# Kernel tuning notes

Measured on AMD Instinct MI355X. Metric: run time of the kernel, lower is better.

The kernel has to match this reference:

```python
import jax, jax.numpy as jnp
import numpy as np

B, T, D, H = 2, 2048, 1024, 16
DH = D // H
TOPK = 64


def setup_inputs() -> dict:
    key = jax.random.key(0)
    ks = jax.random.split(key, 10)
    s = D ** -0.5
    x = jax.random.normal(ks[0], (B, T, D), dtype=jnp.float32)
    key_padding_mask = jax.random.bernoulli(ks[1], 0.1, (B, T))
    Wq = jax.random.normal(ks[2], (D, D), dtype=jnp.float32) * s
    bq = jnp.zeros((D,), dtype=jnp.float32)
    Wk = jax.random.normal(ks[3], (D, D), dtype=jnp.float32) * s
    bk = jnp.zeros((D,), dtype=jnp.float32)
    Wv = jax.random.normal(ks[4], (D, D), dtype=jnp.float32) * s
    bv = jnp.zeros((D,), dtype=jnp.float32)
    Wo = jax.random.normal(ks[5], (D, D), dtype=jnp.float32) * s
    bo = jnp.zeros((D,), dtype=jnp.float32)
    return {"x": x, "Wq": Wq, "bq": bq, "Wk": Wk, "bk": bk,
            "Wv": Wv, "bv": bv, "Wo": Wo, "bo": bo,
            "key_padding_mask": key_padding_mask, "causal": 1}


def _attention(x, Wq, bq, Wk, bk, Wv, bv, Wo, bo, key_padding_mask, causal):
    b, t, d = x.shape
    dh = d // H

    def heads(y):  # (B,T,D) -> (B,H,T,Dh)
        return y.reshape(b, t, H, dh).transpose(0, 2, 1, 3)

    q = heads(x @ Wq.T + bq)
    k = heads(x @ Wk.T + bk)
    v = heads(x @ Wv.T + bv)

    scale = dh ** -0.5
    logits = jnp.einsum('bhqd,bhkd->bhqk', q, k) * scale  # (B,H,T,T)
    neg = jnp.finfo(logits.dtype).min

    # key padding mask: True blocks key position
    logits = jnp.where(key_padding_mask[:, None, None, :], neg, logits)

    if causal:
        i = jnp.arange(t)[:, None]
        j = jnp.arange(t)[None, :]
        blocked = j > (t - t + i)  # Tq == Tk
        logits = jnp.where(blocked[None, None], neg, logits)

    # hard top-k sparsification: keep top-k logits per row, rest -> -inf
    flat = logits.reshape(-1, t)  # (B*H*T, T)
    vals, idx = jax.lax.top_k(flat, TOPK)
    rows = jnp.arange(flat.shape[0])[:, None]
    sparse = jnp.full_like(flat, neg).at[rows, idx].set(vals)
    sparse = sparse.reshape(logits.shape)

    attn = jax.nn.softmax(sparse, axis=-1)
    out = jnp.einsum('bhqk,bhkd->bhqd', attn, v)  # (B,H,T,Dh)
    out = out.transpose(0, 2, 1, 3).reshape(b, t, d)
    return out @ Wo.T + bo


def reference(x, Wq, bq, Wk, bk, Wv, bv, Wo, bo, key_padding_mask, causal):
    return _attention(x, Wq, bq, Wk, bk, Wv, bv, Wo, bo, key_padding_mask, causal)
```

## Files before the change

### kernel.cpp

```cpp
#include <hip/hip_runtime.h>
#include <hip/hip_bf16.h>
#include <stdint.h>

#define BB 2
#define TT 2048
#define DD 1024
#define NH 16
#define HD 64
#define TOPK 64
#define NEGF (-3.402823466e38f)
#define ORD_NEG 0x00800000u
#define QT 16
#define KT 256
#define SELCAP 96

typedef short short8x __attribute__((ext_vector_type(8)));
typedef float floatx4 __attribute__((ext_vector_type(4)));

__device__ __forceinline__ uint32_t ord_u32(float x) {
    uint32_t b = __float_as_uint(x);
    return (b & 0x80000000u) ? ~b : (b | 0x80000000u);
}
__device__ __forceinline__ float unord(uint32_t u) {
    uint32_t b = (u & 0x80000000u) ? (u ^ 0x80000000u) : ~u;
    return __uint_as_float(b);
}
__device__ __forceinline__ short bf16_rne(float x) {
    uint32_t u = __float_as_uint(x);
    u += 0x7FFFu + ((u >> 16) & 1u);
    return (short)(u >> 16);
}
__device__ __forceinline__ float bf16_to_f(short h) {
    return __uint_as_float(((uint32_t)(uint16_t)h) << 16);
}
__device__ __forceinline__ bool mask_at(const void* m, int mode, int idx) {
    if (mode == 0) return ((const int*)m)[idx] != 0;
    if (mode == 1) return ((const unsigned char*)m)[idx] != 0;
    return ((const float*)m)[idx] != 0.0f;
}

__device__ __forceinline__ int dpp_wsum(int v) {
    v += __builtin_amdgcn_update_dpp(0, v, 0x111, 0xf, 0xf, true);
    v += __builtin_amdgcn_update_dpp(0, v, 0x112, 0xf, 0xf, true);
    v += __builtin_amdgcn_update_dpp(0, v, 0x114, 0xf, 0xf, true);
    v += __builtin_amdgcn_update_dpp(0, v, 0x118, 0xf, 0xf, true);
    v += __builtin_amdgcn_update_dpp(0, v, 0x142, 0xa, 0xf, true);
    v += __builtin_amdgcn_update_dpp(0, v, 0x143, 0xc, 0xf, true);
    return __builtin_amdgcn_readlane(v, 63);
}
__device__ __forceinline__ uint32_t dpp_wumax(uint32_t v) {
    uint32_t t;
    t = (uint32_t)__builtin_amdgcn_update_dpp(0, (int)v, 0x111, 0xf, 0xf, true); v = v > t ? v : t;
    t = (uint32_t)__builtin_amdgcn_update_dpp(0, (int)v, 0x112, 0xf, 0xf, true); v = v > t ? v : t;
    t = (uint32_t)__builtin_amdgcn_update_dpp(0, (int)v, 0x114, 0xf, 0xf, true); v = v > t ? v : t;
    t = (uint32_t)__builtin_amdgcn_update_dpp(0, (int)v, 0x118, 0xf, 0xf, true); v = v > t ? v : t;
    t = (uint32_t)__builtin_amdgcn_update_dpp(0, (int)v, 0x142, 0xa, 0xf, true); v = v > t ? v : t;
    t = (uint32_t)__builtin_amdgcn_update_dpp(0, (int)v, 0x143, 0xc, 0xf, true); v = v > t ? v : t;
    return (uint32_t)__builtin_amdgcn_readlane((int)v, 63);
}
__device__ __forceinline__ float dpp_fsum(float v) {
    v += __uint_as_float((uint32_t)__builtin_amdgcn_update_dpp(0, (int)__float_as_uint(v), 0x111, 0xf, 0xf, true));
    v += __uint_as_float((uint32_t)__builtin_amdgcn_update_dpp(0, (int)__float_as_uint(v), 0x112, 0xf, 0xf, true));
    v += __uint_as_float((uint32_t)__builtin_amdgcn_update_dpp(0, (int)__float_as_uint(v), 0x114, 0xf, 0xf, true));
    v += __uint_as_float((uint32_t)__builtin_amdgcn_update_dpp(0, (int)__float_as_uint(v), 0x118, 0xf, 0xf, true));
    v += __uint_as_float((uint32_t)__builtin_amdgcn_update_dpp(0, (int)__float_as_uint(v), 0x142, 0xa, 0xf, true));
    v += __uint_as_float((uint32_t)__builtin_amdgcn_update_dpp(0, (int)__float_as_uint(v), 0x143, 0xc, 0xf, true));
    return __uint_as_float((uint32_t)__builtin_amdgcn_readlane((int)__float_as_uint(v), 63));
}

__global__ void __launch_bounds__(1024) build_flags(
    const unsigned char* raw, const int* causalp, int* flags, uint32_t* Mt)
{
    __shared__ int odd_nz, big, s_mode;
    __shared__ uint32_t smt[BB * 64];
    const int tid = threadIdx.x;
    if (tid == 0) { odd_nz = 0; big = 0; }
    if (tid < BB * 64) smt[tid] = 0;
    __syncthreads();
    for (int i = tid; i < BB * TT; i += 1024) {
        unsigned char c = raw[i];
        if ((i & 3) && c) atomicOr(&odd_nz, 1);
        if (c > 1) atomicOr(&big, 1);
    }
    __syncthreads();
    if (tid == 0) {
        int mode = odd_nz ? (big ? 2 : 1) : 0;
        s_mode = mode;
        flags[0] = mode;
        flags[1] = (causalp[0] != 0) ? 1 : 0;
    }
    __syncthreads();
    const int mode = s_mode;
    const int w = tid >> 3, g = tid & 7;
    const int bb = w >> 6, l = w & 63;
    uint32_t bits = 0;
#pragma unroll
    for (int si = 0; si < 4; ++si) {
        int s = g * 4 + si;
        if (mask_at(raw, mode, bb * TT + l + 64 * s)) bits |= (1u << s);
    }
    if (bits) atomicOr(&smt[w], bits);
    __syncthreads();
    if (tid < BB * 64) Mt[tid] = smt[tid];
}

__global__ void __launch_bounds__(256) split_f32(
    const float* __restrict__ in, short* __restrict__ hi, short* __restrict__ lo,
    int n4, float scale)
{
    int i = blockIdx.x * blockDim.x + threadIdx.x;
    if (i >= n4) return;
    float4 v = ((const float4*)in)[i];
    float f[4] = {v.x * scale, v.y * scale, v.z * scale, v.w * scale};
    short hh[4], ll[4];
#pragma unroll
    for (int j = 0; j < 4; ++j) {
        hh[j] = bf16_rne(f[j]);
        ll[j] = bf16_rne(f[j] - bf16_to_f(hh[j]));
    }
    short4 h4; h4.x = hh[0]; h4.y = hh[1]; h4.z = hh[2]; h4.w = hh[3];
    short4 l4; l4.x = ll[0]; l4.y = ll[1]; l4.z = ll[2]; l4.w = ll[3];
    ((short4*)hi)[i] = h4;
    ((short4*)lo)[i] = l4;
}

__global__ void __launch_bounds__(256) split_w4(
    const float* __restrict__ W0, const float* __restrict__ W1,
    const float* __restrict__ W2, const float* __restrict__ W3,
    short* __restrict__ h0, short* __restrict__ l0, short* __restrict__ h1, short* __restrict__ l1,
    short* __restrict__ h2, short* __restrict__ l2, short* __restrict__ h3, short* __restrict__ l3,
    int n4)
{
    int i = blockIdx.x * blockDim.x + threadIdx.x;
    if (i >= n4) return;
    const int w = blockIdx.y;
    const float* in = (w == 0) ? W0 : (w == 1) ? W1 : (w == 2) ? W2 : W3;
    short* hi = (w == 0) ? h0 : (w == 1) ? h1 : (w == 2) ? h2 : h3;
    short* lo = (w == 0) ? l0 : (w == 1) ? l1 : (w == 2) ? l2 : l3;
    float4 v = ((const float4*)in)[i];
    float f[4] = {v.x, v.y, v.z, v.w};
    short hh[4], ll[4];
#pragma unroll
    for (int j = 0; j < 4; ++j) {
        hh[j] = bf16_rne(f[j]);
        ll[j] = bf16_rne(f[j] - bf16_to_f(hh[j]));
    }
    short4 h4; h4.x = hh[0]; h4.y = hh[1]; h4.z = hh[2]; h4.w = hh[3];
    short4 l4; l4.x = ll[0]; l4.y = ll[1]; l4.z = ll[2]; l4.w = ll[3];
    ((short4*)hi)[i] = h4;
    ((short4*)lo)[i] = l4;
}

__global__ void __launch_bounds__(256) gemm_bf16s(
    const short* __restrict__ Ah, const short* __restrict__ Al,
    const short* __restrict__ Bh, const short* __restrict__ Bl,
    const float* __restrict__ bias, float* __restrict__ Cf,
    short* __restrict__ Ch, short* __restrict__ Cl, float scale, int mode)
{
    const int bid = blockIdx.x;
    const int xcd = bid & 7, slot = bid >> 3;
    const int panel = xcd * 4 + (slot >> 4);
    const int ncol  = slot & 15;
    const int tid = threadIdx.x, lane = tid & 63, wv = tid >> 6;
    const int wr = wv >> 1, wc = wv & 1;
    const int m0 = panel * 128 + wr * 64;
    const int n0 = ncol * 64 + wc * 32;
    const int lrow = lane & 15, lk = (lane >> 4) * 8;

    floatx4 acc[4][2];
#pragma unroll
    for (int i = 0; i < 4; ++i)
#pragma unroll
        for (int j = 0; j < 2; ++j) acc[i][j] = (floatx4){0.f, 0.f, 0.f, 0.f};

    auto ldfr = [&](int kk, short8x* pah, short8x* pal, short8x* pbh, short8x* pbl) {
#pragma unroll
        for (int mb = 0; mb < 4; ++mb) {
            size_t off = (size_t)(m0 + mb * 16 + lrow) * DD + kk + lk;
            pah[mb] = *(const short8x*)(Ah + off);
            pal[mb] = *(const short8x*)(Al + off);
        }
#pragma unroll
        for (int nb = 0; nb < 2; ++nb) {
            size_t off = (size_t)(n0 + nb * 16 + lrow) * DD + kk + lk;
            pbh[nb] = *(const short8x*)(Bh + off);
            pbl[nb] = *(const short8x*)(Bl + off);
        }
    };
    auto domfma = [&](short8x* pah, short8x* pal, short8x* pbh, short8x* pbl) {
#pragma unroll
        for (int mb = 0; mb < 4; ++mb)
#pragma unroll
            for (int nb = 0; nb < 2; ++nb) {
                acc[mb][nb] = __builtin_amdgcn_mfma_f32_16x16x32_bf16(pah[mb], pbh[nb], acc[mb][nb], 0, 0, 0);
                acc[mb][nb] = __builtin_amdgcn_mfma_f32_16x16x32_bf16(pah[mb], pbl[nb], acc[mb][nb], 0, 0, 0);
                acc[mb][nb] = __builtin_amdgcn_mfma_f32_16x16x32_bf16(pal[mb], pbh[nb], acc[mb][nb], 0, 0, 0);
            }
    };

    short8x A0[4], L0[4], B0[2], C0[2];
    short8x A1[4], L1[4], B1[2], C1[2];
    ldfr(0, A0, L0, B0, C0);
    for (int kk = 0; kk < DD; kk += 64) {
        ldfr(kk + 32, A1, L1, B1, C1);
        domfma(A0, L0, B0, C0);
        if (kk + 64 < DD) ldfr(kk + 64, A0, L0, B0, C0);
        domfma(A1, L1, B1, C1);
    }

#pragma unroll
    for (int mb = 0; mb < 4; ++mb)
#pragma unroll
        for (int nb = 0; nb < 2; ++nb) {
            int n = n0 + nb * 16 + lrow;
            float bv = bias[n];
#pragma unroll
            for (int j = 0; j < 4; ++j) {
                int m = m0 + mb * 16 + (lane >> 4) * 4 + j;
                float v = acc[mb][nb][j] + bv;
                if (mode == 0) {
                    Cf[(size_t)m * DD + n] = v;
                } else {
                    int b = m >> 11, t = m & (TT - 1), h = n >> 6, dh = n & (HD - 1);
                    size_t idx = (((size_t)b * NH + h) * TT + t) * HD + dh;
                    if (mode == 1) {
                        Cf[idx] = v;
                    } else {
                        v *= scale;
                        short hi16 = bf16_rne(v);
                        Ch[idx] = hi16;
                        Cl[idx] = bf16_rne(v - bf16_to_f(hi16));
                    }
                }
            }
        }
}

__global__ void __launch_bounds__(256) gemm_xwt(
    const float* __restrict__ A, const float* __restrict__ W,
    const float* __restrict__ bias, float* __restrict__ C,
    int M, int N, int K, int split_heads)
{
    __shared__ float As[64][17];
    __shared__ float Ws[64][17];
    const int tid = threadIdx.x;
    const int tx = tid & 15, ty = tid >> 4;
    const int arow = blockIdx.y * 64, bcol = blockIdx.x * 64;
    float acc[4][4] = {};

    for (int k0 = 0; k0 < K; k0 += 16) {
        const int r = tid >> 2, c = (tid & 3) * 4;
        float4 a4 = *(const float4*)(A + (size_t)(arow + r) * K + k0 + c);
        As[r][c] = a4.x; As[r][c + 1] = a4.y; As[r][c + 2] = a4.z; As[r][c + 3] = a4.w;
        float4 w4 = *(const float4*)(W + (size_t)(bcol + r) * K + k0 + c);
        Ws[r][c] = w4.x; Ws[r][c + 1] = w4.y; Ws[r][c + 2] = w4.z; Ws[r][c + 3] = w4.w;
        __syncthreads();
#pragma unroll
        for (int k = 0; k < 16; ++k) {
            float a0 = As[ty * 4 + 0][k], a1 = As[ty * 4 + 1][k];
            float a2 = As[ty * 4 + 2][k], a3 = As[ty * 4 + 3][k];
            float w0 = Ws[tx * 4 + 0][k], w1 = Ws[tx * 4 + 1][k];
            float w2 = Ws[tx * 4 + 2][k], w3 = Ws[tx * 4 + 3][k];
            acc[0][0] += a0 * w0; acc[0][1] += a0 * w1; acc[0][2] += a0 * w2; acc[0][3] += a0 * w3;
            acc[1][0] += a1 * w0; acc[1][1] += a1 * w1; acc[1][2] += a1 * w2; acc[1][3] += a1 * w3;
            acc[2][0] += a2 * w0; acc[2][1] += a2 * w1; acc[2][2] += a2 * w2; acc[2][3] += a2 * w3;
            acc[3][0] += a3 * w0; acc[3][1] += a3 * w1; acc[3][2] += a3 * w2; acc[3][3] += a3 * w3;
        }
        __syncthreads();
    }

#pragma unroll
    for (int i = 0; i < 4; ++i) {
        int m = arow + ty * 4 + i;
#pragma unroll
        for (int j = 0; j < 4; ++j) {
            int n = bcol + tx * 4 + j;
            float v = acc[i][j] + bias[n];
            if (split_heads) {
                int b = m / TT, t = m % TT, h = n / HD, dh = n % HD;
                C[(((size_t)b * NH + h) * TT + t) * HD + dh] = v;
            } else {
                C[(size_t)m * N + n] = v;
            }
        }
    }
}

__global__ void __launch_bounds__(1024) attn_topk(
    const short* __restrict__ Qhi, const short* __restrict__ Qlo,
    const short* __restrict__ Khi, const short* __restrict__ Klo,
    const float* __restrict__ V, const uint32_t* __restrict__ Mt,
    const int* __restrict__ flags, short* __restrict__ Ohi,
    short* __restrict__ Olo, float* __restrict__ Of)
{
    __shared__ float s_S[2][QT][KT + 1];
    __shared__ int2  s_sel[QT][SELCAP];

    const int tid = threadIdx.x, lane = tid & 63, wv = tid >> 6;
    const int d = blockIdx.x;
    const int xcd = d & 7, chunk = d >> 3;
    const int bh = (xcd << 2) | (chunk >> 7);
    const int qt = chunk & 127;
    const int b = bh >> 4, h = bh & 15;
    const int causal = flags[1];
    const size_t hb = (size_t)bh * (size_t)TT * HD;
    const int r0 = qt * QT;
    const int gq = r0 + wv;
    const float* __restrict__ Vh = V + hb;
    const float* __restrict__ Vl = Vh + lane;

    short8x qhi[2], qlo[2];
    {
        const size_t qoff = hb + (size_t)(r0 + (lane & 15)) * HD + (lane >> 4) * 8;
        qhi[0] = *(const short8x*)(Qhi + qoff);
        qhi[1] = *(const short8x*)(Qhi + qoff + 32);
        qlo[0] = *(const short8x*)(Qlo + qoff);
        qlo[1] = *(const short8x*)(Qlo + qoff + 32);
    }

    const uint32_t mwords = Mt[b * 64 + lane];

    uint32_t lgo[32];
#pragma unroll
    for (int i = 0; i < 32; ++i) lgo[i] = ORD_NEG;

    const int lastT = causal ? ((r0 + QT - 1) >> 8) : 7;

#pragma unroll
    for (int t = 0; t < 8; ++t) {
        if (t <= lastT) {
            const size_t koff = hb + (size_t)(t * KT + wv * 16 + (lane & 15)) * HD + (lane >> 4) * 8;
            short8x kh0 = *(const short8x*)(Khi + koff);
            short8x kh1 = *(const short8x*)(Khi + koff + 32);
            short8x kl0 = *(const short8x*)(Klo + koff);
            short8x kl1 = *(const short8x*)(Klo + koff + 32);
            floatx4 acc = {0.f, 0.f, 0.f, 0.f};
            acc = __builtin_amdgcn_mfma_f32_16x16x32_bf16(qhi[0], kh0, acc, 0, 0, 0);
            acc = __builtin_amdgcn_mfma_f32_16x16x32_bf16(qhi[0], kl0, acc, 0, 0, 0);
            acc = __builtin_amdgcn_mfma_f32_16x16x32_bf16(qlo[0], kh0, acc, 0, 0, 0);
            acc = __builtin_amdgcn_mfma_f32_16x16x32_bf16(qhi[1], kh1, acc, 0, 0, 0);
            acc = __builtin_amdgcn_mfma_f32_16x16x32_bf16(qhi[1], kl1, acc, 0, 0, 0);
            acc = __builtin_amdgcn_mfma_f32_16x16x32_bf16(qlo[1], kh1, acc, 0, 0, 0);
#pragma unroll
            for (int j = 0; j < 4; ++j)
                s_S[t & 1][(lane >> 4) * 4 + j][wv * 16 + (lane & 15)] = acc[j];
            __syncthreads();
#pragma unroll
            for (int j = 0; j < 4; ++j) {
                float sv = s_S[t & 1][wv][j * 64 + lane];
                int key = t * KT + j * 64 + lane;
                bool blocked = ((mwords >> (t * 4 + j)) & 1u) || (causal && key > gq);
                lgo[t * 4 + j] = blocked ? ORD_NEG : ord_u32(sv);
            }
        }
    }

    uint32_t moL = 0;
#pragma unroll
    for (int i = 0; i < 32; ++i) {
        uint32_t u = lgo[i];
        moL = u > moL ? u : moL;
    }
    const uint32_t mo = dpp_wumax(moL);

    auto wcount = [&](uint32_t thrv) -> int {
        int c = 0;
#pragma unroll
        for (int i = 0; i < 32; ++i) c += (lgo[i] >= thrv) ? 1 : 0;
        return dpp_wsum(c);
    };

    float outv;
    if (mo == ORD_NEG) {
        float a0 = 0.f, a1 = 0.f, a2 = 0.f, a3 = 0.f;
        for (int j = 0; j < TT; j += 4) {
            a0 += Vh[(j + 0) * HD + lane];
            a1 += Vh[(j + 1) * HD + lane];
            a2 += Vh[(j + 2) * HD + lane];
            a3 += Vh[(j + 3) * HD + lane];
        }
        outv = (a0 + a1 + a2 + a3) * (1.0f / TT);
    } else {
        const float mF = unord(mo);
        uint32_t thr = 0; uint32_t lo_b = 0, hi_b = 0; int done = 0;
        {
            uint32_t p1 = ord_u32(mF - 2.0f);
            int c1 = wcount(p1);
            if (c1 == TOPK) { thr = p1; done = 1; }
            else if (c1 > TOPK) { lo_b = p1; hi_b = mo; }
            else {
                uint32_t p2 = ord_u32(mF - 4.0f);
                int c2 = wcount(p2);
                if (c2 == TOPK) { thr = p2; done = 1; }
                else if (c2 > TOPK) { lo_b = p2; hi_b = p1; }
                else {
                    uint32_t p3 = ord_u32(mF - 15.0f);
                    int c3 = wcount(p3);
                    if (c3 <= TOPK) { thr = p3; done = 1; }
                    else { lo_b = p3; hi_b = p2; }
                }
            }
        }
        if (!done) {
            while (hi_b - lo_b > 1u) {
                uint32_t mid = lo_b + ((hi_b - lo_b) >> 1);
                int c = wcount(mid);
                if (c == TOPK) { lo_b = mid; break; }
                if (c > TOPK) lo_b = mid; else hi_b = mid;
            }
            thr = lo_b;
        }

        float Sp = 0.f;
#pragma unroll
        for (int i = 0; i < 32; ++i) {
            uint32_t u = lgo[i];
            float w = 0.f;
            if (u >= thr) w = __expf(unord(u) - mF);
            Sp += w;
            lgo[i] = (w > 0.f) ? __float_as_uint(w) : 0u;
        }
        const float S = dpp_fsum(Sp);

        int base = 0;
#pragma unroll
        for (int i = 0; i < 32; ++i) {
            uint32_t wbits = lgo[i];
            unsigned long long msk = __ballot(wbits != 0);
            if (wbits) {
                int below = __builtin_amdgcn_mbcnt_hi((uint32_t)(msk >> 32),
                            __builtin_amdgcn_mbcnt_lo((uint32_t)msk, 0));
                int pos = base + below;
                if (pos < SELCAP) {
                    int keyoff = (((i >> 2) * KT + (i & 3) * 64 + lane) << 6);
                    s_sel[wv][pos] = make_int2(keyoff, (int)wbits);
                }
            }
            base += (int)__popcll(msk);
        }
        int cnt = base < SELCAP ? base : SELCAP;

        float acc = 0.f;
        int i2 = 0;
        for (; i2 + 4 <= cnt; i2 += 4) {
            int2 e0 = s_sel[wv][i2],     e1 = s_sel[wv][i2 + 1];
            int2 e2 = s_sel[wv][i2 + 2], e3 = s_sel[wv][i2 + 3];
            int k0 = __builtin_amdgcn_readfirstlane(e0.x);
            int k1 = __builtin_amdgcn_readfirstlane(e1.x);
            int k2 = __builtin_amdgcn_readfirstlane(e2.x);
            int k3 = __builtin_amdgcn_readfirstlane(e3.x);
            float w0 = __uint_as_float((uint32_t)__builtin_amdgcn_readfirstlane(e0.y));
            float w1 = __uint_as_float((uint32_t)__builtin_amdgcn_readfirstlane(e1.y));
            float w2 = __uint_as_float((uint32_t)__builtin_amdgcn_readfirstlane(e2.y));
            float w3 = __uint_as_float((uint32_t)__builtin_amdgcn_readfirstlane(e3.y));
            acc += w0 * Vl[k0];
            acc += w1 * Vl[k1];
            acc += w2 * Vl[k2];
            acc += w3 * Vl[k3];
        }
        for (; i2 < cnt; ++i2) {
            int2 e = s_sel[wv][i2];
            int k = __builtin_amdgcn_readfirstlane(e.x);
            float w = __uint_as_float((uint32_t)__builtin_amdgcn_readfirstlane(e.y));
            acc += w * Vl[k];
        }
        outv = acc / S;
    }
    const size_t oidx = ((size_t)b * TT + gq) * DD + h * HD + lane;
    if (Of) {
        Of[oidx] = outv;
    } else {
        short hi16 = bf16_rne(outv);
        Ohi[oidx] = hi16;
        Olo[oidx] = bf16_rne(outv - bf16_to_f(hi16));
    }
}

extern "C" void kernel_launch(void* const* d_in, const int* in_sizes, int n_in,
                              void* d_out, int out_size, void* d_ws, size_t ws_size,
                              hipStream_t stream) {
    const float* x  = (const float*)d_in[0];
    const float* Wq = (const float*)d_in[1];
    const float* bq = (const float*)d_in[2];
    const float* Wk = (const float*)d_in[3];
    const float* bk = (const float*)d_in[4];
    const float* Wv = (const float*)d_in[5];
    const float* bv = (const float*)d_in[6];
    const float* Wo = (const float*)d_in[7];
    const float* bo = (const float*)d_in[8];
    const void*  maskp = d_in[9];
    const int*   causalp = (const int*)d_in[10];
    float* out = (float*)d_out;

    char* ws = (char*)d_ws;
    const size_t TEN  = (size_t)BB * TT * DD * sizeof(float);
    const size_t HTEN = TEN / 2;
    const size_t WSZ  = (size_t)DD * DD * 2;
    const size_t NEED = 6 * TEN + 4096;

    const int nx4 = BB * TT * DD / 4, nw4 = DD * DD / 4;

    if (ws_size >= NEED) {
        float* Vf   = (float*)(ws);
        short* xh   = (short*)(ws + TEN);
        short* xl   = (short*)(ws + TEN + HTEN);
        short* Qhi  = (short*)(ws + 2 * TEN);
        short* Qlo  = (short*)(ws + 2 * TEN + HTEN);
        short* Khi  = (short*)(ws + 3 * TEN);
        short* Klo  = (short*)(ws + 3 * TEN + HTEN);
        short* Ohi  = (short*)(ws + 4 * TEN);
        short* Olo  = (short*)(ws + 4 * TEN + HTEN);
        char*  wb   = ws + 5 * TEN;
        short* wqh = (short*)(wb);            short* wql = (short*)(wb + WSZ);
        short* wkh = (short*)(wb + 2 * WSZ);  short* wkl = (short*)(wb + 3 * WSZ);
        short* wvh = (short*)(wb + 4 * WSZ);  short* wvl = (short*)(wb + 5 * WSZ);
        short* woh = (short*)(wb + 6 * WSZ);  short* wol = (short*)(wb + 7 * WSZ);
        int*      flags = (int*)(wb + 8 * WSZ);
        uint32_t* Mt    = (uint32_t*)(wb + 8 * WSZ + 256);

        build_flags<<<1, 1024, 0, stream>>>((const unsigned char*)maskp, causalp, flags, Mt);

        split_f32<<<(nx4 + 255) / 256, 256, 0, stream>>>(x, xh, xl, nx4, 1.0f);
        dim3 wg((nw4 + 255) / 256, 4);
        split_w4<<<wg, 256, 0, stream>>>(Wq, Wk, Wv, Wo,
                                         wqh, wql, wkh, wkl, wvh, wvl, woh, wol, nw4);

        gemm_bf16s<<<512, 256, 0, stream>>>(xh, xl, wqh, wql, bq, nullptr, Qhi, Qlo, 0.125f, 2);
        gemm_bf16s<<<512, 256, 0, stream>>>(xh, xl, wkh, wkl, bk, nullptr, Khi, Klo, 1.0f, 2);
        gemm_bf16s<<<512, 256, 0, stream>>>(xh, xl, wvh, wvl, bv, Vf, nullptr, nullptr, 1.0f, 1);

        attn_topk<<<BB * NH * (TT / QT), 1024, 0, stream>>>(Qhi, Qlo, Khi, Klo, Vf, Mt, flags,
                                                            Ohi, Olo, nullptr);

        gemm_bf16s<<<512, 256, 0, stream>>>(Ohi, Olo, woh, wol, bo, out, nullptr, nullptr, 1.0f, 0);
    } else {
        float* Qf  = (float*)(ws);
        float* Kf  = (float*)(ws + TEN);
        float* Vf  = (float*)(ws + 2 * TEN);
        float* O   = (float*)(ws + 3 * TEN);
        short* Qhi = (short*)(ws + 4 * TEN);
        short* Qlo = (short*)(ws + 4 * TEN + HTEN);
        short* Khi = (short*)(ws + 5 * TEN);
        short* Klo = (short*)(ws + 5 * TEN + HTEN);
        int*      flags = (int*)(ws + 6 * TEN);
        uint32_t* Mt    = (uint32_t*)(ws + 6 * TEN + 256);

        build_flags<<<1, 1024, 0, stream>>>((const unsigned char*)maskp, causalp, flags, Mt);
        dim3 g2(DD / 64, (BB * TT) / 64);
        gemm_xwt<<<g2, 256, 0, stream>>>(x, Wq, bq, Qf, BB * TT, DD, DD, 1);
        gemm_xwt<<<g2, 256, 0, stream>>>(x, Wk, bk, Kf, BB * TT, DD, DD, 1);
        gemm_xwt<<<g2, 256, 0, stream>>>(x, Wv, bv, Vf, BB * TT, DD, DD, 1);
        split_f32<<<(nx4 + 255) / 256, 256, 0, stream>>>(Qf, Qhi, Qlo, nx4, 0.125f);
        split_f32<<<(nx4 + 255) / 256, 256, 0, stream>>>(Kf, Khi, Klo, nx4, 1.0f);
        attn_topk<<<BB * NH * (TT / QT), 1024, 0, stream>>>(Qhi, Qlo, Khi, Klo, Vf, Mt, flags,
                                                            nullptr, nullptr, O);
        gemm_xwt<<<g2, 256, 0, stream>>>(O, Wo, bo, out, BB * TT, DD, DD, 0);
    }
}
```

Before: 770.4 us.

## Fuse QKV GEMMs, drop split-bf16 for V and output projections

Merges the three Q/K/V projection GEMMs into one 1536-block launch. The V projection and the output projection now use a single bf16 MFMA term instead of the three-term hi/lo split, and the attention output is stored as bf16 only. In the attention kernel the count uses ballot/popcount, and the softmax weights are computed only for the selected keys, with weights and keys held in registers and read back via readlane instead of broadcast LDS reads. This cuts MFMA work and memory traffic in two of the GEMMs, at the cost of lower precision in the V and output projections.

```diff
diff --git a/kernel.cpp b/kernel.cpp
--- a/kernel.cpp
+++ b/kernel.cpp
@@ -39,15 +39,6 @@
     return ((const float*)m)[idx] != 0.0f;
 }
 
-__device__ __forceinline__ int dpp_wsum(int v) {
-    v += __builtin_amdgcn_update_dpp(0, v, 0x111, 0xf, 0xf, true);
-    v += __builtin_amdgcn_update_dpp(0, v, 0x112, 0xf, 0xf, true);
-    v += __builtin_amdgcn_update_dpp(0, v, 0x114, 0xf, 0xf, true);
-    v += __builtin_amdgcn_update_dpp(0, v, 0x118, 0xf, 0xf, true);
-    v += __builtin_amdgcn_update_dpp(0, v, 0x142, 0xa, 0xf, true);
-    v += __builtin_amdgcn_update_dpp(0, v, 0x143, 0xc, 0xf, true);
-    return __builtin_amdgcn_readlane(v, 63);
-}
 __device__ __forceinline__ uint32_t dpp_wumax(uint32_t v) {
     uint32_t t;
     t = (uint32_t)__builtin_amdgcn_update_dpp(0, (int)v, 0x111, 0xf, 0xf, true); v = v > t ? v : t;
@@ -151,11 +142,104 @@
     ((short4*)lo)[i] = l4;
 }
 
+__global__ void __launch_bounds__(256) gemm_qkv(
+    const short* __restrict__ Ah, const short* __restrict__ Al,
+    const short* __restrict__ Wqh, const short* __restrict__ Wql,
+    const short* __restrict__ Wkh, const short* __restrict__ Wkl,
+    const short* __restrict__ Wvh,
+    const float* __restrict__ bq, const float* __restrict__ bk, const float* __restrict__ bv,
+    short* __restrict__ Qhi, short* __restrict__ Qlo,
+    short* __restrict__ Khi, short* __restrict__ Klo, float* __restrict__ Vf)
+{
+    const int bid = blockIdx.x;
+    const int xcd = bid & 7, slot = bid >> 3;
+    const int panel = xcd * 4 + slot / 48;
+    const int nc48  = slot % 48;
+    const int wsel  = nc48 >> 4;
+    const int ncol  = nc48 & 15;
+    const int tid = threadIdx.x, lane = tid & 63, wv = tid >> 6;
+    const int wr = wv >> 1, wc = wv & 1;
+    const int m0 = panel * 128 + wr * 64;
+    const int n0 = ncol * 64 + wc * 32;
+    const int lrow = lane & 15, lk = (lane >> 4) * 8;
+
+    const short* Bh = (wsel == 0) ? Wqh : (wsel == 1) ? Wkh : Wvh;
+    const short* Bl = (wsel == 0) ? Wql : Wkl;
+    const float* bias = (wsel == 0) ? bq : (wsel == 1) ? bk : bv;
+    const int terms = (wsel == 2) ? 0 : 3;
+
+    floatx4 acc[4][2];
+#pragma unroll
+    for (int i = 0; i < 4; ++i)
+#pragma unroll
+        for (int j = 0; j < 2; ++j) acc[i][j] = (floatx4){0.f, 0.f, 0.f, 0.f};
+
+    auto ldfr = [&](int kk, short8x* pah, short8x* pal, short8x* pbh, short8x* pbl) {
+#pragma unroll
+        for (int mb = 0; mb < 4; ++mb) {
+            size_t off = (size_t)(m0 + mb * 16 + lrow) * DD + kk + lk;
+            pah[mb] = *(const short8x*)(Ah + off);
+            if (terms) pal[mb] = *(const short8x*)(Al + off);
+        }
+#pragma unroll
+        for (int nb = 0; nb < 2; ++nb) {
+            size_t off = (size_t)(n0 + nb * 16 + lrow) * DD + kk + lk;
+            pbh[nb] = *(const short8x*)(Bh + off);
+            if (terms) pbl[nb] = *(const short8x*)(Bl + off);
+        }
+    };
+    auto domfma = [&](short8x* pah, short8x* pal, short8x* pbh, short8x* pbl) {
+#pragma unroll
+        for (int mb = 0; mb < 4; ++mb)
+#pragma unroll
+            for (int nb = 0; nb < 2; ++nb) {
+                acc[mb][nb] = __builtin_amdgcn_mfma_f32_16x16x32_bf16(pah[mb], pbh[nb], acc[mb][nb], 0, 0, 0);
+                if (terms) {
+                    acc[mb][nb] = __builtin_amdgcn_mfma_f32_16x16x32_bf16(pah[mb], pbl[nb], acc[mb][nb], 0, 0, 0);
+                    acc[mb][nb] = __builtin_amdgcn_mfma_f32_16x16x32_bf16(pal[mb], pbh[nb], acc[mb][nb], 0, 0, 0);
+                }
+            }
+    };
+
+    short8x A0[4], L0[4], B0[2], C0[2];
+    short8x A1[4], L1[4], B1[2], C1[2];
+    ldfr(0, A0, L0, B0, C0);
+    for (int kk = 0; kk < DD; kk += 64) {
+        ldfr(kk + 32, A1, L1, B1, C1);
+        domfma(A0, L0, B0, C0);
+        if (kk + 64 < DD) ldfr(kk + 64, A0, L0, B0, C0);
+        domfma(A1, L1, B1, C1);
+    }
+
+    const float scale = (wsel == 0) ? 0.125f : 1.0f;
+#pragma unroll
+    for (int mb = 0; mb < 4; ++mb)
+#pragma unroll
+        for (int nb = 0; nb < 2; ++nb) {
+            int n = n0 + nb * 16 + lrow;
+            float bv2 = bias[n];
+#pragma unroll
+            for (int j = 0; j < 4; ++j) {
+                int m = m0 + mb * 16 + (lane >> 4) * 4 + j;
+                float v = acc[mb][nb][j] + bv2;
+                int b = m >> 11, t = m & (TT - 1), h = n >> 6, dh = n & (HD - 1);
+                size_t idx = (((size_t)b * NH + h) * TT + t) * HD + dh;
+                if (wsel == 2) {
+                    Vf[idx] = v;
+                } else {
+                    v *= scale;
+                    short hi16 = bf16_rne(v);
+                    short lo16 = bf16_rne(v - bf16_to_f(hi16));
+                    if (wsel == 0) { Qhi[idx] = hi16; Qlo[idx] = lo16; }
+                    else           { Khi[idx] = hi16; Klo[idx] = lo16; }
+                }
+            }
+        }
+}
+
 __global__ void __launch_bounds__(256) gemm_bf16s(
-    const short* __restrict__ Ah, const short* __restrict__ Al,
-    const short* __restrict__ Bh, const short* __restrict__ Bl,
-    const float* __restrict__ bias, float* __restrict__ Cf,
-    short* __restrict__ Ch, short* __restrict__ Cl, float scale, int mode)
+    const short* __restrict__ Ah, const short* __restrict__ Bh,
+    const float* __restrict__ bias, float* __restrict__ Cf)
 {
     const int bid = blockIdx.x;
     const int xcd = bid & 7, slot = bid >> 3;
@@ -173,39 +257,29 @@
 #pragma unroll
         for (int j = 0; j < 2; ++j) acc[i][j] = (floatx4){0.f, 0.f, 0.f, 0.f};
 
-    auto ldfr = [&](int kk, short8x* pah, short8x* pal, short8x* pbh, short8x* pbl) {
-#pragma unroll
-        for (int mb = 0; mb < 4; ++mb) {
-            size_t off = (size_t)(m0 + mb * 16 + lrow) * DD + kk + lk;
-            pah[mb] = *(const short8x*)(Ah + off);
-            pal[mb] = *(const short8x*)(Al + off);
-        }
-#pragma unroll
-        for (int nb = 0; nb < 2; ++nb) {
-            size_t off = (size_t)(n0 + nb * 16 + lrow) * DD + kk + lk;
-            pbh[nb] = *(const short8x*)(Bh + off);
-            pbl[nb] = *(const short8x*)(Bl + off);
-        }
+    auto ldfr = [&](int kk, short8x* pah, short8x* pbh) {
+#pragma unroll
+        for (int mb = 0; mb < 4; ++mb)
+            pah[mb] = *(const short8x*)(Ah + (size_t)(m0 + mb * 16 + lrow) * DD + kk + lk);
+#pragma unroll
+        for (int nb = 0; nb < 2; ++nb)
+            pbh[nb] = *(const short8x*)(Bh + (size_t)(n0 + nb * 16 + lrow) * DD + kk + lk);
     };
-    auto domfma = [&](short8x* pah, short8x* pal, short8x* pbh, short8x* pbl) {
+    auto domfma = [&](short8x* pah, short8x* pbh) {
 #pragma unroll
         for (int mb = 0; mb < 4; ++mb)
 #pragma unroll
-            for (int nb = 0; nb < 2; ++nb) {
+            for (int nb = 0; nb < 2; ++nb)
                 acc[mb][nb] = __builtin_amdgcn_mfma_f32_16x16x32_bf16(pah[mb], pbh[nb], acc[mb][nb], 0, 0, 0);
-                acc[mb][nb] = __builtin_amdgcn_mfma_f32_16x16x32_bf16(pah[mb], pbl[nb], acc[mb][nb], 0, 0, 0);
-                acc[mb][nb] = __builtin_amdgcn_mfma_f32_16x16x32_bf16(pal[mb], pbh[nb], acc[mb][nb], 0, 0, 0);
-            }
     };
 
-    short8x A0[4], L0[4], B0[2], C0[2];
-    short8x A1[4], L1[4], B1[2], C1[2];
-    ldfr(0, A0, L0, B0, C0);
+    short8x A0[4], B0[2], A1[4], B1[2];
+    ldfr(0, A0, B0);
     for (int kk = 0; kk < DD; kk += 64) {
-        ldfr(kk + 32, A1, L1, B1, C1);
-        domfma(A0, L0, B0, C0);
-        if (kk + 64 < DD) ldfr(kk + 64, A0, L0, B0, C0);
-        domfma(A1, L1, B1, C1);
+        ldfr(kk + 32, A1, B1);
+        domfma(A0, B0);
+        if (kk + 64 < DD) ldfr(kk + 64, A0, B0);
+        domfma(A1, B1);
     }
 
 #pragma unroll
@@ -217,21 +291,7 @@
 #pragma unroll
             for (int j = 0; j < 4; ++j) {
                 int m = m0 + mb * 16 + (lane >> 4) * 4 + j;
-                float v = acc[mb][nb][j] + bv;
-                if (mode == 0) {
-                    Cf[(size_t)m * DD + n] = v;
-                } else {
-                    int b = m >> 11, t = m & (TT - 1), h = n >> 6, dh = n & (HD - 1);
-                    size_t idx = (((size_t)b * NH + h) * TT + t) * HD + dh;
-                    if (mode == 1) {
-                        Cf[idx] = v;
-                    } else {
-                        v *= scale;
-                        short hi16 = bf16_rne(v);
-                        Ch[idx] = hi16;
-                        Cl[idx] = bf16_rne(v - bf16_to_f(hi16));
-                    }
-                }
+                Cf[(size_t)m * DD + n] = acc[mb][nb][j] + bv;
             }
         }
 }
@@ -291,7 +351,7 @@
     const short* __restrict__ Khi, const short* __restrict__ Klo,
     const float* __restrict__ V, const uint32_t* __restrict__ Mt,
     const int* __restrict__ flags, short* __restrict__ Ohi,
-    short* __restrict__ Olo, float* __restrict__ Of)
+    float* __restrict__ Of)
 {
     __shared__ float s_S[2][QT][KT + 1];
     __shared__ int2  s_sel[QT][SELCAP];
@@ -366,8 +426,9 @@
     auto wcount = [&](uint32_t thrv) -> int {
         int c = 0;
 #pragma unroll
-        for (int i = 0; i < 32; ++i) c += (lgo[i] >= thrv) ? 1 : 0;
-        return dpp_wsum(c);
+        for (int i = 0; i < 32; ++i)
+            c += (int)__popcll(__ballot(lgo[i] >= thrv));
+        return c;
     };
 
     float outv;
@@ -411,69 +472,69 @@
             thr = lo_b;
         }
 
-        float Sp = 0.f;
+        int base = 0;
 #pragma unroll
         for (int i = 0; i < 32; ++i) {
             uint32_t u = lgo[i];
-            float w = 0.f;
-            if (u >= thr) w = __expf(unord(u) - mF);
-            Sp += w;
-            lgo[i] = (w > 0.f) ? __float_as_uint(w) : 0u;
-        }
-        const float S = dpp_fsum(Sp);
-
-        int base = 0;
-#pragma unroll
-        for (int i = 0; i < 32; ++i) {
-            uint32_t wbits = lgo[i];
-            unsigned long long msk = __ballot(wbits != 0);
-            if (wbits) {
+            unsigned long long msk = __ballot(u >= thr);
+            if (u >= thr) {
                 int below = __builtin_amdgcn_mbcnt_hi((uint32_t)(msk >> 32),
                             __builtin_amdgcn_mbcnt_lo((uint32_t)msk, 0));
                 int pos = base + below;
                 if (pos < SELCAP) {
                     int keyoff = (((i >> 2) * KT + (i & 3) * 64 + lane) << 6);
-                    s_sel[wv][pos] = make_int2(keyoff, (int)wbits);
+                    s_sel[wv][pos] = make_int2(keyoff, (int)u);
                 }
             }
             base += (int)__popcll(msk);
         }
-        int cnt = base < SELCAP ? base : SELCAP;
+        const int cnt = base < SELCAP ? base : SELCAP;
+
+        float w0r = 0.f, w1r = 0.f; int key0r = 0, key1r = 0;
+        if (lane < cnt) {
+            int2 e = s_sel[wv][lane];
+            key0r = e.x;
+            w0r = __expf(unord((uint32_t)e.y) - mF);
+        }
+        if (64 + lane < cnt) {
+            int2 e = s_sel[wv][64 + lane];
+            key1r = e.x;
+            w1r = __expf(unord((uint32_t)e.y) - mF);
+        }
+        const float S = dpp_fsum(w0r + w1r);
 
         float acc = 0.f;
-        int i2 = 0;
-        for (; i2 + 4 <= cnt; i2 += 4) {
-            int2 e0 = s_sel[wv][i2],     e1 = s_sel[wv][i2 + 1];
-            int2 e2 = s_sel[wv][i2 + 2], e3 = s_sel[wv][i2 + 3];
-            int k0 = __builtin_amdgcn_readfirstlane(e0.x);
-            int k1 = __builtin_amdgcn_readfirstlane(e1.x);
-            int k2 = __builtin_amdgcn_readfirstlane(e2.x);
-            int k3 = __builtin_amdgcn_readfirstlane(e3.x);
-            float w0 = __uint_as_float((uint32_t)__builtin_amdgcn_readfirstlane(e0.y));
-            float w1 = __uint_as_float((uint32_t)__builtin_amdgcn_readfirstlane(e1.y));
-            float w2 = __uint_as_float((uint32_t)__builtin_amdgcn_readfirstlane(e2.y));
-            float w3 = __uint_as_float((uint32_t)__builtin_amdgcn_readfirstlane(e3.y));
-            acc += w0 * Vl[k0];
-            acc += w1 * Vl[k1];
-            acc += w2 * Vl[k2];
-            acc += w3 * Vl[k3];
-        }
-        for (; i2 < cnt; ++i2) {
-            int2 e = s_sel[wv][i2];
-            int k = __builtin_amdgcn_readfirstlane(e.x);
-            float w = __uint_as_float((uint32_t)__builtin_amdgcn_readfirstlane(e.y));
-            acc += w * Vl[k];
+        const int c0 = cnt < 64 ? cnt : 64;
+        int k = 0;
+        for (; k + 4 <= c0; k += 4) {
+            int ka = __builtin_amdgcn_readlane(key0r, k);
+            int kb = __builtin_amdgcn_readlane(key0r, k + 1);
+            int kc = __builtin_amdgcn_readlane(key0r, k + 2);
+            int kd = __builtin_amdgcn_readlane(key0r, k + 3);
+            float wa = __uint_as_float((uint32_t)__builtin_amdgcn_readlane((int)__float_as_uint(w0r), k));
+            float wb = __uint_as_float((uint32_t)__builtin_amdgcn_readlane((int)__float_as_uint(w0r), k + 1));
+            float wc = __uint_as_float((uint32_t)__builtin_amdgcn_readlane((int)__float_as_uint(w0r), k + 2));
+            float wd = __uint_as_float((uint32_t)__builtin_amdgcn_readlane((int)__float_as_uint(w0r), k + 3));
+            acc += wa * Vl[ka];
+            acc += wb * Vl[kb];
+            acc += wc * Vl[kc];
+            acc += wd * Vl[kd];
+        }
+        for (; k < c0; ++k) {
+            int kk2 = __builtin_amdgcn_readlane(key0r, k);
+            float wk2 = __uint_as_float((uint32_t)__builtin_amdgcn_readlane((int)__float_as_uint(w0r), k));
+            acc += wk2 * Vl[kk2];
+        }
+        for (k = 64; k < cnt; ++k) {
+            int kk2 = __builtin_amdgcn_readlane(key1r, k - 64);
+            float wk2 = __uint_as_float((uint32_t)__builtin_amdgcn_readlane((int)__float_as_uint(w1r), k - 64));
+            acc += wk2 * Vl[kk2];
         }
         outv = acc / S;
     }
     const size_t oidx = ((size_t)b * TT + gq) * DD + h * HD + lane;
-    if (Of) {
-        Of[oidx] = outv;
-    } else {
-        short hi16 = bf16_rne(outv);
-        Ohi[oidx] = hi16;
-        Olo[oidx] = bf16_rne(outv - bf16_to_f(hi16));
-    }
+    if (Of) Of[oidx] = outv;
+    else    Ohi[oidx] = bf16_rne(outv);
 }
 
 extern "C" void kernel_launch(void* const* d_in, const int* in_sizes, int n_in,
@@ -509,7 +570,6 @@
         short* Khi  = (short*)(ws + 3 * TEN);
         short* Klo  = (short*)(ws + 3 * TEN + HTEN);
         short* Ohi  = (short*)(ws + 4 * TEN);
-        short* Olo  = (short*)(ws + 4 * TEN + HTEN);
         char*  wb   = ws + 5 * TEN;
         short* wqh = (short*)(wb);            short* wql = (short*)(wb + WSZ);
         short* wkh = (short*)(wb + 2 * WSZ);  short* wkl = (short*)(wb + 3 * WSZ);
@@ -525,14 +585,13 @@
         split_w4<<<wg, 256, 0, stream>>>(Wq, Wk, Wv, Wo,
                                          wqh, wql, wkh, wkl, wvh, wvl, woh, wol, nw4);
 
-        gemm_bf16s<<<512, 256, 0, stream>>>(xh, xl, wqh, wql, bq, nullptr, Qhi, Qlo, 0.125f, 2);
-        gemm_bf16s<<<512, 256, 0, stream>>>(xh, xl, wkh, wkl, bk, nullptr, Khi, Klo, 1.0f, 2);
-        gemm_bf16s<<<512, 256, 0, stream>>>(xh, xl, wvh, wvl, bv, Vf, nullptr, nullptr, 1.0f, 1);
+        gemm_qkv<<<1536, 256, 0, stream>>>(xh, xl, wqh, wql, wkh, wkl, wvh,
+                                           bq, bk, bv, Qhi, Qlo, Khi, Klo, Vf);
 
         attn_topk<<<BB * NH * (TT / QT), 1024, 0, stream>>>(Qhi, Qlo, Khi, Klo, Vf, Mt, flags,
-                                                            Ohi, Olo, nullptr);
-
-        gemm_bf16s<<<512, 256, 0, stream>>>(Ohi, Olo, woh, wol, bo, out, nullptr, nullptr, 1.0f, 0);
+                                                            Ohi, nullptr);
+
+        gemm_bf16s<<<512, 256, 0, stream>>>(Ohi, woh, bo, out);
     } else {
         float* Qf  = (float*)(ws);
         float* Kf  = (float*)(ws + TEN);
@@ -553,7 +612,7 @@
         split_f32<<<(nx4 + 255) / 256, 256, 0, stream>>>(Qf, Qhi, Qlo, nx4, 0.125f);
         split_f32<<<(nx4 + 255) / 256, 256, 0, stream>>>(Kf, Khi, Klo, nx4, 1.0f);
         attn_topk<<<BB * NH * (TT / QT), 1024, 0, stream>>>(Qhi, Qlo, Khi, Klo, Vf, Mt, flags,
-                                                            nullptr, nullptr, O);
+                                                            nullptr, O);
         gemm_xwt<<<g2, 256, 0, stream>>>(O, Wo, bo, out, BB * TT, DD, DD, 0);
     }
 }
```

Result: faster. 710.6 us (-7.8%).
